# Optimization experiments

Measured on AMD Instinct MI355X. Metric: run time of the kernel, lower is better.

## Reference

```python
import jax, jax.numpy as jnp
import numpy as np

B, N, H, F_IN, F_OUT = 16, 512, 8, 128, 128
NEG_SLOPE = 0.2


def setup_inputs() -> dict:
    key = jax.random.key(0)
    k_h, k_adj, k_bias, k_W, k_a = jax.random.split(key, 5)
    h = jax.random.normal(k_h, (B, N, F_IN), dtype=jnp.float32)
    # Binary adjacency (shared across batch); force self-loops so every row
    # of the masked softmax has at least one valid entry (avoids NaN rows).
    adj = jax.random.randint(k_adj, (N, N), 0, 2, dtype=jnp.int32)
    adj = adj.at[jnp.arange(N), jnp.arange(N)].set(1)
    bias_matrix = jax.random.normal(k_bias, (1, 1, N, N), dtype=jnp.float32)
    # Xavier-uniform-like init for params
    lim_W = float(np.sqrt(6.0 / (F_IN + F_OUT)))
    W = jax.random.uniform(k_W, (H, F_IN, F_OUT), minval=-lim_W, maxval=lim_W, dtype=jnp.float32)
    lim_a = float(np.sqrt(6.0 / (2 * F_OUT + 1)))
    a = jax.random.uniform(k_a, (H, 2 * F_OUT, 1), minval=-lim_a, maxval=lim_a, dtype=jnp.float32)
    return {"h": h, "adj": adj, "bias_matrix": bias_matrix, "W": W, "a": a}


def reference(h, adj, bias_matrix, W, a):
    # h: [B,N,Fin], adj: [N,N] int, bias_matrix: [1,1,N,N], W: [H,Fin,F], a: [H,2F,1]
    f = W.shape[-1]
    h_prime = jnp.einsum('bni,hio->bnho', h, W)  # [B,N,H,F]
    # e[b,i,j,h] = leakyrelu(a_h . concat(h_prime[b,i,h], h_prime[b,j,h]))
    # Decompose a into src/dst halves: identical math, avoids O(B*N*N*H*2F) cat.
    a_src = a[:, :f, 0]  # [H,F]
    a_dst = a[:, f:, 0]  # [H,F]
    s_src = jnp.einsum('bnhf,hf->bnh', h_prime, a_src)  # score contribution of node i
    s_dst = jnp.einsum('bnhf,hf->bnh', h_prime, a_dst)  # score contribution of node j
    e = jax.nn.leaky_relu(s_src[:, :, None, :] + s_dst[:, None, :, :], NEG_SLOPE)  # [B,N,N,H]
    e = e + bias_matrix[0, 0][None, :, :, None]  # bias broadcast over batch & heads
    mask = (adj != 0)[None, :, :, None]  # [1,N,N,1] -> broadcast [B,N,N,H]
    e = jnp.where(mask, e, -jnp.inf)
    attention = jax.nn.softmax(e, axis=2)  # softmax over neighbors j
    h_out = jnp.einsum('bijh,bjhf->bihf', attention, h_prime)  # [B,N,H,F]
    # concat=False -> mean over heads
    return h_out.mean(axis=2)  # [B,N,F]
```

## Files before the change

kernel.cpp:

```cpp
#include <hip/hip_runtime.h>
#include <hip/hip_bf16.h>
#include <string.h>

#define NB 16
#define NN 512
#define NH 8
#define NF 128
#define NEG_SLOPE 0.2f

typedef short bf16x8 __attribute__((ext_vector_type(8)));
typedef float f32x4 __attribute__((ext_vector_type(4)));

__device__ inline unsigned short f2bf(float x) {
    unsigned int u = __float_as_uint(x);
    unsigned int r = (u + 0x7fffu + ((u >> 16) & 1u)) >> 16;
    return (unsigned short)r;
}

__global__ __launch_bounds__(256) void prep_kernel(
    const int* __restrict__ adj, const float* __restrict__ bias,
    const float* __restrict__ W, const float* __restrict__ a,
    float* __restrict__ mb, float* __restrict__ wasrc, float* __restrict__ wadst)
{
    int t = blockIdx.x * 256 + threadIdx.x;
    if (t < NN * NN) mb[t] = (adj[t] != 0) ? bias[t] : -1.0e30f;
    if (t < NH * NF) {
        int hh = t >> 7, i = t & 127;
        const float* wrow = W + (hh * NF + i) * NF;
        const float* asr = a + hh * 2 * NF;
        const float* ads = asr + NF;
        float s1 = 0.f, s2 = 0.f;
        #pragma unroll 4
        for (int f = 0; f < NF; ++f) {
            float w = wrow[f];
            s1 = fmaf(w, asr[f], s1);
            s2 = fmaf(w, ads[f], s2);
        }
        wasrc[t] = s1; wadst[t] = s2;
    }
}

__global__ __launch_bounds__(256) void score_kernel(
    const float* __restrict__ h, const float* __restrict__ wasrc,
    const float* __restrict__ wadst, float* __restrict__ ssrc, float* __restrict__ sdstT)
{
    __shared__ float wsm[2][NH * (NF + 4)];
    int tid = threadIdx.x;
    for (int u = tid; u < NH * NF; u += 256) {
        int hh = u >> 7, f = u & 127;
        wsm[0][hh * (NF + 4) + f] = wasrc[u];
        wsm[1][hh * (NF + 4) + f] = wadst[u];
    }
    __syncthreads();
    int t = blockIdx.x * 256 + tid;
    int hh = t & 7;
    int bn = t >> 3;
    int b = bn >> 9, n = bn & 511;
    const float4* hrow = (const float4*)(h + (size_t)bn * NF);
    const float4* w1 = (const float4*)(&wsm[0][hh * (NF + 4)]);
    const float4* w2 = (const float4*)(&wsm[1][hh * (NF + 4)]);
    float s1 = 0.f, s2 = 0.f;
    #pragma unroll
    for (int u = 0; u < NF / 4; ++u) {
        float4 hv = hrow[u], a1 = w1[u], a2 = w2[u];
        s1 += hv.x * a1.x + hv.y * a1.y + hv.z * a1.z + hv.w * a1.w;
        s2 += hv.x * a2.x + hv.y * a2.y + hv.z * a2.z + hv.w * a2.w;
    }
    ssrc[t] = s1;
    sdstT[((size_t)(b * NH + hh)) * NN + n] = s2;
}

__global__ __launch_bounds__(256) void hprime_kernel(
    const float* __restrict__ h, const float* __restrict__ W, unsigned short* __restrict__ hpT)
{
    __shared__ float As[64][NF + 4];
    __shared__ float Ws[NF][64];
    int tid = threadIdx.x;
    int rowBase = blockIdx.x * 64;
    int colBase = blockIdx.y * 64;
    int hh = colBase >> 7;
    int fbase = colBase & 127;
    {
        int r = tid >> 2, kc = (tid & 3) * 32;
        const float4* src = (const float4*)(h + (size_t)(rowBase + r) * NF + kc);
        #pragma unroll
        for (int u = 0; u < 8; ++u)
            *(float4*)&As[r][kc + 4 * u] = src[u];
    }
    {
        int c = (tid & 15) * 4;
        int k0 = tid >> 4;
        #pragma unroll
        for (int u = 0; u < 8; ++u) {
            int k = k0 + u * 16;
            *(float4*)&Ws[k][c] = *(const float4*)(W + (size_t)(hh * NF + k) * NF + fbase + c);
        }
    }
    __syncthreads();
    int tx = tid & 15, ty = tid >> 4;
    float acc[4][4];
    #pragma unroll
    for (int r = 0; r < 4; ++r)
        #pragma unroll
        for (int c = 0; c < 4; ++c) acc[r][c] = 0.f;
    #pragma unroll 4
    for (int k = 0; k < NF; ++k) {
        float4 wv = *(const float4*)&Ws[k][tx * 4];
        float av[4];
        av[0] = As[ty * 4 + 0][k];
        av[1] = As[ty * 4 + 1][k];
        av[2] = As[ty * 4 + 2][k];
        av[3] = As[ty * 4 + 3][k];
        #pragma unroll
        for (int r = 0; r < 4; ++r) {
            acc[r][0] = fmaf(av[r], wv.x, acc[r][0]);
            acc[r][1] = fmaf(av[r], wv.y, acc[r][1]);
            acc[r][2] = fmaf(av[r], wv.z, acc[r][2]);
            acc[r][3] = fmaf(av[r], wv.w, acc[r][3]);
        }
    }
    int b = rowBase >> 9;
    int nInB = (rowBase & 511) + ty * 4;
    #pragma unroll
    for (int cc = 0; cc < 4; ++cc) {
        int f = fbase + tx * 4 + cc;
        ushort4 u;
        u.x = f2bf(acc[0][cc]);
        u.y = f2bf(acc[1][cc]);
        u.z = f2bf(acc[2][cc]);
        u.w = f2bf(acc[3][cc]);
        *(ushort4*)&hpT[((size_t)(b * NH + hh) * NF + f) * NN + nInB] = u;
    }
}

__global__ __launch_bounds__(1024, 4) void attn_kernel(
    const unsigned short* __restrict__ hpT, const float* __restrict__ mb,
    const float* __restrict__ ssrc, const float* __restrict__ sdstT,
    float* __restrict__ out)
{
    __shared__ float mbs[32][NN];
    __shared__ unsigned short P[32][NN + 8];

    int i0 = (blockIdx.x & 15) * 32;
    int b  = blockIdx.x >> 4;
    int tid = threadIdx.x;
    int lane = tid & 63, wave = tid >> 6;

    for (int u = tid; u < 32 * (NN / 4); u += 1024) {
        int r = u >> 7, c4 = (u & 127) * 4;
        *(float4*)&mbs[r][c4] = *(const float4*)&mb[(size_t)(i0 + r) * NN + c4];
    }
    __syncthreads();

    int iGrp = wave >> 3;
    int fch  = wave & 7;
    f32x4 acc0 = {0.f, 0.f, 0.f, 0.f};
    f32x4 acc1 = {0.f, 0.f, 0.f, 0.f};

    for (int hh = 0; hh < NH; ++hh) {
        const float* sd = sdstT + ((size_t)(b * NH + hh)) * NN;
        #pragma unroll
        for (int rr = 0; rr < 2; ++rr) {
            int i = wave * 2 + rr;
            int row = i0 + i;
            float s_i = ssrc[((size_t)(b * NN + row)) * NH + hh];
            float p8[8];
            float mx = -3.0e38f;
            #pragma unroll
            for (int v = 0; v < 8; ++v) {
                int j = lane + 64 * v;
                float x = s_i + sd[j];
                x = x > 0.f ? x : NEG_SLOPE * x;
                float e = x + mbs[i][j];
                p8[v] = e;
                mx = fmaxf(mx, e);
            }
            #pragma unroll
            for (int off = 32; off; off >>= 1) mx = fmaxf(mx, __shfl_xor(mx, off));
            float sum = 0.f;
            #pragma unroll
            for (int v = 0; v < 8; ++v) { p8[v] = __expf(p8[v] - mx); sum += p8[v]; }
            #pragma unroll
            for (int off = 32; off; off >>= 1) sum += __shfl_xor(sum, off);
            float rinv = 1.0f / sum;
            #pragma unroll
            for (int v = 0; v < 8; ++v)
                P[i][lane + 64 * v] = f2bf(p8[v] * rinv);
        }
        __syncthreads();

        const unsigned short* Bp = hpT
            + ((size_t)(b * NH + hh) * NF + fch * 16 + (lane & 15)) * NN
            + (lane >> 4) * 8;
        const unsigned short* Ap = &P[iGrp * 16 + (lane & 15)][(lane >> 4) * 8];
        #pragma unroll
        for (int ks = 0; ks < 16; ks += 2) {
            bf16x8 a0 = *(const bf16x8*)(Ap + ks * 32);
            bf16x8 b0 = *(const bf16x8*)(Bp + ks * 32);
            acc0 = __builtin_amdgcn_mfma_f32_16x16x32_bf16(a0, b0, acc0, 0, 0, 0);
            bf16x8 a1 = *(const bf16x8*)(Ap + (ks + 1) * 32);
            bf16x8 b1 = *(const bf16x8*)(Bp + (ks + 1) * 32);
            acc1 = __builtin_amdgcn_mfma_f32_16x16x32_bf16(a1, b1, acc1, 0, 0, 0);
        }
        __syncthreads();
    }

    int f = fch * 16 + (lane & 15);
    int ibase = i0 + iGrp * 16 + (lane >> 4) * 4;
    #pragma unroll
    for (int r = 0; r < 4; ++r)
        out[((size_t)(b * NN + ibase + r)) * NF + f] = (acc0[r] + acc1[r]) * 0.125f;
}

extern "C" void kernel_launch(void* const* d_in, const int* in_sizes, int n_in,
                              void* d_out, int out_size, void* d_ws, size_t ws_size,
                              hipStream_t stream)
{
    const float* h    = (const float*)d_in[0];
    const int*   adj  = (const int*)d_in[1];
    const float* bias = (const float*)d_in[2];
    const float* W    = (const float*)d_in[3];
    const float* a    = (const float*)d_in[4];
    float* out = (float*)d_out;

    unsigned short* hpT = (unsigned short*)d_ws;
    float* mb    = (float*)(hpT + (size_t)NB * NH * NF * NN);
    float* ssrc  = mb + (size_t)NN * NN;
    float* sdstT = ssrc + (size_t)NB * NN * NH;
    float* wasrc = sdstT + (size_t)NB * NN * NH;
    float* wadst = wasrc + NH * NF;

    hipLaunchKernelGGL(prep_kernel, dim3((NN * NN) / 256), dim3(256), 0, stream,
                       adj, bias, W, a, mb, wasrc, wadst);
    hipLaunchKernelGGL(score_kernel, dim3((NB * NN * NH) / 256), dim3(256), 0, stream,
                       h, wasrc, wadst, ssrc, sdstT);
    hipLaunchKernelGGL(hprime_kernel, dim3((NB * NN) / 64, (NH * NF) / 64), dim3(256), 0, stream,
                       h, W, hpT);
    hipLaunchKernelGGL(attn_kernel, dim3(NB * (NN / 32)), dim3(1024), 0, stream,
                       hpT, mb, ssrc, sdstT, out);
}
```

Before: 193.3 us.

## Use split-bf16 MFMA for h' projection and split attention over head halves

Adds a split kernel that stores h and transposed W as hi/lo bf16 pairs. The h' projection now runs as three-pass bf16 MFMA (hi*hi, lo*hi, hi*lo) instead of a scalar fp32 FMA GEMM, which shifts that compute onto the matrix cores. The attention kernel now uses 16-row tiles with 512 threads, splits the 8 heads across two blocks that write partial sums, and loads the bias/mask directly from global with vectorized reads instead of staging it in LDS. It also prefetches B fragments and adds a combine kernel, which costs two extra launches and extra global traffic for the hi/lo buffers and the partial outputs.

```diff
diff --git a/kernel.cpp b/kernel.cpp
--- a/kernel.cpp
+++ b/kernel.cpp
@@ -1,6 +1,5 @@
 #include <hip/hip_runtime.h>
 #include <hip/hip_bf16.h>
-#include <string.h>
 
 #define NB 16
 #define NN 512
@@ -9,12 +8,16 @@
 #define NEG_SLOPE 0.2f
 
 typedef short bf16x8 __attribute__((ext_vector_type(8)));
+typedef unsigned short u16x8 __attribute__((ext_vector_type(8)));
 typedef float f32x4 __attribute__((ext_vector_type(4)));
 
 __device__ inline unsigned short f2bf(float x) {
     unsigned int u = __float_as_uint(x);
     unsigned int r = (u + 0x7fffu + ((u >> 16) & 1u)) >> 16;
     return (unsigned short)r;
+}
+__device__ inline float bf2f(unsigned short u) {
+    return __uint_as_float(((unsigned int)u) << 16);
 }
 
 __global__ __launch_bounds__(256) void prep_kernel(
@@ -40,6 +43,29 @@
     }
 }
 
+__global__ __launch_bounds__(256) void split_kernel(
+    const float* __restrict__ h, const float* __restrict__ W,
+    unsigned short* __restrict__ hHi, unsigned short* __restrict__ hLo,
+    unsigned short* __restrict__ wtHi, unsigned short* __restrict__ wtLo)
+{
+    int t = blockIdx.x * 256 + threadIdx.x;
+    if (t < NB * NN * NF) {
+        float v = h[t];
+        unsigned short hi = f2bf(v);
+        hHi[t] = hi;
+        hLo[t] = f2bf(v - bf2f(hi));
+    } else {
+        int u = t - NB * NN * NF;
+        if (u < NH * NF * NF) {
+            int fg = u >> 7, k = u & 127;
+            float v = W[(size_t)(fg >> 7) * NF * NF + k * NF + (fg & 127)];
+            unsigned short hi = f2bf(v);
+            wtHi[u] = hi;
+            wtLo[u] = f2bf(v - bf2f(hi));
+        }
+    }
+}
+
 __global__ __launch_bounds__(256) void score_kernel(
     const float* __restrict__ h, const float* __restrict__ wasrc,
     const float* __restrict__ wadst, float* __restrict__ ssrc, float* __restrict__ sdstT)
@@ -71,110 +97,114 @@
 }
 
 __global__ __launch_bounds__(256) void hprime_kernel(
-    const float* __restrict__ h, const float* __restrict__ W, unsigned short* __restrict__ hpT)
-{
-    __shared__ float As[64][NF + 4];
-    __shared__ float Ws[NF][64];
+    const unsigned short* __restrict__ hHi, const unsigned short* __restrict__ hLo,
+    const unsigned short* __restrict__ wtHi, const unsigned short* __restrict__ wtLo,
+    unsigned short* __restrict__ hpT)
+{
     int tid = threadIdx.x;
-    int rowBase = blockIdx.x * 64;
-    int colBase = blockIdx.y * 64;
-    int hh = colBase >> 7;
-    int fbase = colBase & 127;
-    {
-        int r = tid >> 2, kc = (tid & 3) * 32;
-        const float4* src = (const float4*)(h + (size_t)(rowBase + r) * NF + kc);
-        #pragma unroll
-        for (int u = 0; u < 8; ++u)
-            *(float4*)&As[r][kc + 4 * u] = src[u];
-    }
-    {
-        int c = (tid & 15) * 4;
-        int k0 = tid >> 4;
-        #pragma unroll
-        for (int u = 0; u < 8; ++u) {
-            int k = k0 + u * 16;
-            *(float4*)&Ws[k][c] = *(const float4*)(W + (size_t)(hh * NF + k) * NF + fbase + c);
-        }
-    }
-    __syncthreads();
-    int tx = tid & 15, ty = tid >> 4;
-    float acc[4][4];
+    int wave = tid >> 6, lane = tid & 63;
+    int col = lane & 15, kg = lane >> 4;
+    int f0 = blockIdx.y * 64 + wave * 16;
+    int n0 = blockIdx.x * 64;
+
+    const unsigned short* Ah = wtHi + (size_t)(f0 + col) * NF + kg * 8;
+    const unsigned short* Al = wtLo + (size_t)(f0 + col) * NF + kg * 8;
+    const unsigned short* Bh0 = hHi + (size_t)(n0 +  0 + col) * NF + kg * 8;
+    const unsigned short* Bh1 = hHi + (size_t)(n0 + 16 + col) * NF + kg * 8;
+    const unsigned short* Bh2 = hHi + (size_t)(n0 + 32 + col) * NF + kg * 8;
+    const unsigned short* Bh3 = hHi + (size_t)(n0 + 48 + col) * NF + kg * 8;
+    const unsigned short* Bl0 = hLo + (size_t)(n0 +  0 + col) * NF + kg * 8;
+    const unsigned short* Bl1 = hLo + (size_t)(n0 + 16 + col) * NF + kg * 8;
+    const unsigned short* Bl2 = hLo + (size_t)(n0 + 32 + col) * NF + kg * 8;
+    const unsigned short* Bl3 = hLo + (size_t)(n0 + 48 + col) * NF + kg * 8;
+
+    f32x4 acc0 = {0.f,0.f,0.f,0.f}, acc1 = {0.f,0.f,0.f,0.f};
+    f32x4 acc2 = {0.f,0.f,0.f,0.f}, acc3 = {0.f,0.f,0.f,0.f};
+
     #pragma unroll
-    for (int r = 0; r < 4; ++r)
-        #pragma unroll
-        for (int c = 0; c < 4; ++c) acc[r][c] = 0.f;
-    #pragma unroll 4
-    for (int k = 0; k < NF; ++k) {
-        float4 wv = *(const float4*)&Ws[k][tx * 4];
-        float av[4];
-        av[0] = As[ty * 4 + 0][k];
-        av[1] = As[ty * 4 + 1][k];
-        av[2] = As[ty * 4 + 2][k];
-        av[3] = As[ty * 4 + 3][k];
-        #pragma unroll
-        for (int r = 0; r < 4; ++r) {
-            acc[r][0] = fmaf(av[r], wv.x, acc[r][0]);
-            acc[r][1] = fmaf(av[r], wv.y, acc[r][1]);
-            acc[r][2] = fmaf(av[r], wv.z, acc[r][2]);
-            acc[r][3] = fmaf(av[r], wv.w, acc[r][3]);
-        }
-    }
-    int b = rowBase >> 9;
-    int nInB = (rowBase & 511) + ty * 4;
+    for (int ks = 0; ks < 4; ++ks) {
+        int off = ks * 32;
+        bf16x8 ahi = *(const bf16x8*)(Ah + off);
+        bf16x8 alo = *(const bf16x8*)(Al + off);
+        bf16x8 b0h = *(const bf16x8*)(Bh0 + off);
+        bf16x8 b1h = *(const bf16x8*)(Bh1 + off);
+        bf16x8 b2h = *(const bf16x8*)(Bh2 + off);
+        bf16x8 b3h = *(const bf16x8*)(Bh3 + off);
+        bf16x8 b0l = *(const bf16x8*)(Bl0 + off);
+        bf16x8 b1l = *(const bf16x8*)(Bl1 + off);
+        bf16x8 b2l = *(const bf16x8*)(Bl2 + off);
+        bf16x8 b3l = *(const bf16x8*)(Bl3 + off);
+        acc0 = __builtin_amdgcn_mfma_f32_16x16x32_bf16(ahi, b0h, acc0, 0, 0, 0);
+        acc1 = __builtin_amdgcn_mfma_f32_16x16x32_bf16(ahi, b1h, acc1, 0, 0, 0);
+        acc2 = __builtin_amdgcn_mfma_f32_16x16x32_bf16(ahi, b2h, acc2, 0, 0, 0);
+        acc3 = __builtin_amdgcn_mfma_f32_16x16x32_bf16(ahi, b3h, acc3, 0, 0, 0);
+        acc0 = __builtin_amdgcn_mfma_f32_16x16x32_bf16(alo, b0h, acc0, 0, 0, 0);
+        acc1 = __builtin_amdgcn_mfma_f32_16x16x32_bf16(alo, b1h, acc1, 0, 0, 0);
+        acc2 = __builtin_amdgcn_mfma_f32_16x16x32_bf16(alo, b2h, acc2, 0, 0, 0);
+        acc3 = __builtin_amdgcn_mfma_f32_16x16x32_bf16(alo, b3h, acc3, 0, 0, 0);
+        acc0 = __builtin_amdgcn_mfma_f32_16x16x32_bf16(ahi, b0l, acc0, 0, 0, 0);
+        acc1 = __builtin_amdgcn_mfma_f32_16x16x32_bf16(ahi, b1l, acc1, 0, 0, 0);
+        acc2 = __builtin_amdgcn_mfma_f32_16x16x32_bf16(ahi, b2l, acc2, 0, 0, 0);
+        acc3 = __builtin_amdgcn_mfma_f32_16x16x32_bf16(ahi, b3l, acc3, 0, 0, 0);
+    }
+
+    int b = n0 >> 9;
+    int nin = n0 & 511;
     #pragma unroll
-    for (int cc = 0; cc < 4; ++cc) {
-        int f = fbase + tx * 4 + cc;
-        ushort4 u;
-        u.x = f2bf(acc[0][cc]);
-        u.y = f2bf(acc[1][cc]);
-        u.z = f2bf(acc[2][cc]);
-        u.w = f2bf(acc[3][cc]);
-        *(ushort4*)&hpT[((size_t)(b * NH + hh) * NF + f) * NN + nInB] = u;
-    }
-}
-
-__global__ __launch_bounds__(1024, 4) void attn_kernel(
+    for (int r = 0; r < 4; ++r) {
+        int fg = f0 + kg * 4 + r;
+        size_t base = ((size_t)b * (NH * NF) + fg) * NN + nin + col;
+        hpT[base +  0] = f2bf(acc0[r]);
+        hpT[base + 16] = f2bf(acc1[r]);
+        hpT[base + 32] = f2bf(acc2[r]);
+        hpT[base + 48] = f2bf(acc3[r]);
+    }
+}
+
+__global__ __launch_bounds__(512, 8) void attn_kernel(
     const unsigned short* __restrict__ hpT, const float* __restrict__ mb,
     const float* __restrict__ ssrc, const float* __restrict__ sdstT,
-    float* __restrict__ out)
-{
-    __shared__ float mbs[32][NN];
-    __shared__ unsigned short P[32][NN + 8];
-
-    int i0 = (blockIdx.x & 15) * 32;
-    int b  = blockIdx.x >> 4;
+    float* __restrict__ part)
+{
+    __shared__ unsigned short P[16][520];
+
+    int bx = blockIdx.x;
+    int half = bx & 1;
+    int it = (bx >> 1) & 31;
+    int b = bx >> 6;
+    int i0 = it * 16;
     int tid = threadIdx.x;
     int lane = tid & 63, wave = tid >> 6;
-
-    for (int u = tid; u < 32 * (NN / 4); u += 1024) {
-        int r = u >> 7, c4 = (u & 127) * 4;
-        *(float4*)&mbs[r][c4] = *(const float4*)&mb[(size_t)(i0 + r) * NN + c4];
-    }
-    __syncthreads();
-
-    int iGrp = wave >> 3;
-    int fch  = wave & 7;
-    f32x4 acc0 = {0.f, 0.f, 0.f, 0.f};
-    f32x4 acc1 = {0.f, 0.f, 0.f, 0.f};
-
-    for (int hh = 0; hh < NH; ++hh) {
-        const float* sd = sdstT + ((size_t)(b * NH + hh)) * NN;
+    int col = lane & 15, kg = lane >> 4;
+
+    f32x4 acc0 = {0.f,0.f,0.f,0.f}, acc1 = {0.f,0.f,0.f,0.f};
+
+    for (int hq = 0; hq < 4; ++hq) {
+        int head = half * 4 + hq;
+        const float* sd = sdstT + (size_t)(b * NH + head) * NN;
         #pragma unroll
         for (int rr = 0; rr < 2; ++rr) {
             int i = wave * 2 + rr;
             int row = i0 + i;
-            float s_i = ssrc[((size_t)(b * NN + row)) * NH + hh];
+            float s_i = ssrc[((size_t)(b * NN + row)) * NH + head];
+            const float4* sd4 = (const float4*)(sd + lane * 8);
+            const float4* mb4 = (const float4*)(mb + (size_t)row * NN + lane * 8);
+            float4 sv0 = sd4[0], sv1 = sd4[1];
+            float4 mv0 = mb4[0], mv1 = mb4[1];
             float p8[8];
-            float mx = -3.0e38f;
-            #pragma unroll
-            for (int v = 0; v < 8; ++v) {
-                int j = lane + 64 * v;
-                float x = s_i + sd[j];
-                x = x > 0.f ? x : NEG_SLOPE * x;
-                float e = x + mbs[i][j];
-                p8[v] = e;
-                mx = fmaxf(mx, e);
+            {
+                float x;
+                x = s_i + sv0.x; x = x > 0.f ? x : NEG_SLOPE * x; p8[0] = x + mv0.x;
+                x = s_i + sv0.y; x = x > 0.f ? x : NEG_SLOPE * x; p8[1] = x + mv0.y;
+                x = s_i + sv0.z; x = x > 0.f ? x : NEG_SLOPE * x; p8[2] = x + mv0.z;
+                x = s_i + sv0.w; x = x > 0.f ? x : NEG_SLOPE * x; p8[3] = x + mv0.w;
+                x = s_i + sv1.x; x = x > 0.f ? x : NEG_SLOPE * x; p8[4] = x + mv1.x;
+                x = s_i + sv1.y; x = x > 0.f ? x : NEG_SLOPE * x; p8[5] = x + mv1.y;
+                x = s_i + sv1.z; x = x > 0.f ? x : NEG_SLOPE * x; p8[6] = x + mv1.z;
+                x = s_i + sv1.w; x = x > 0.f ? x : NEG_SLOPE * x; p8[7] = x + mv1.w;
             }
+            float mx = fmaxf(fmaxf(fmaxf(p8[0], p8[1]), fmaxf(p8[2], p8[3])),
+                             fmaxf(fmaxf(p8[4], p8[5]), fmaxf(p8[6], p8[7])));
             #pragma unroll
             for (int off = 32; off; off >>= 1) mx = fmaxf(mx, __shfl_xor(mx, off));
             float sum = 0.f;
@@ -183,33 +213,53 @@
             #pragma unroll
             for (int off = 32; off; off >>= 1) sum += __shfl_xor(sum, off);
             float rinv = 1.0f / sum;
+            u16x8 pw;
             #pragma unroll
-            for (int v = 0; v < 8; ++v)
-                P[i][lane + 64 * v] = f2bf(p8[v] * rinv);
+            for (int v = 0; v < 8; ++v) pw[v] = f2bf(p8[v] * rinv);
+            *(u16x8*)&P[i][lane * 8] = pw;
         }
         __syncthreads();
 
         const unsigned short* Bp = hpT
-            + ((size_t)(b * NH + hh) * NF + fch * 16 + (lane & 15)) * NN
-            + (lane >> 4) * 8;
-        const unsigned short* Ap = &P[iGrp * 16 + (lane & 15)][(lane >> 4) * 8];
+            + ((size_t)(b * NH + head) * NF + wave * 16 + col) * NN + kg * 8;
+        const unsigned short* Ap = &P[col][kg * 8];
+        bf16x8 B0v = *(const bf16x8*)(Bp);
+        bf16x8 B1v = *(const bf16x8*)(Bp + 32);
         #pragma unroll
-        for (int ks = 0; ks < 16; ks += 2) {
-            bf16x8 a0 = *(const bf16x8*)(Ap + ks * 32);
-            bf16x8 b0 = *(const bf16x8*)(Bp + ks * 32);
-            acc0 = __builtin_amdgcn_mfma_f32_16x16x32_bf16(a0, b0, acc0, 0, 0, 0);
-            bf16x8 a1 = *(const bf16x8*)(Ap + (ks + 1) * 32);
-            bf16x8 b1 = *(const bf16x8*)(Bp + (ks + 1) * 32);
-            acc1 = __builtin_amdgcn_mfma_f32_16x16x32_bf16(a1, b1, acc1, 0, 0, 0);
+        for (int ks = 0; ks < 8; ++ks) {
+            bf16x8 a0 = *(const bf16x8*)(Ap + ks * 64);
+            bf16x8 a1 = *(const bf16x8*)(Ap + ks * 64 + 32);
+            bf16x8 nb0, nb1;
+            if (ks < 7) {
+                nb0 = *(const bf16x8*)(Bp + ks * 64 + 64);
+                nb1 = *(const bf16x8*)(Bp + ks * 64 + 96);
+            }
+            acc0 = __builtin_amdgcn_mfma_f32_16x16x32_bf16(a0, B0v, acc0, 0, 0, 0);
+            acc1 = __builtin_amdgcn_mfma_f32_16x16x32_bf16(a1, B1v, acc1, 0, 0, 0);
+            if (ks < 7) { B0v = nb0; B1v = nb1; }
         }
         __syncthreads();
     }
 
-    int f = fch * 16 + (lane & 15);
-    int ibase = i0 + iGrp * 16 + (lane >> 4) * 4;
+    float* po = part + (size_t)half * (NB * NN * NF);
     #pragma unroll
-    for (int r = 0; r < 4; ++r)
-        out[((size_t)(b * NN + ibase + r)) * NF + f] = (acc0[r] + acc1[r]) * 0.125f;
+    for (int r = 0; r < 4; ++r) {
+        po[((size_t)(b * NN + i0 + kg * 4 + r)) * NF + wave * 16 + col] = acc0[r] + acc1[r];
+    }
+}
+
+__global__ __launch_bounds__(256) void combine_kernel(
+    const float* __restrict__ part, float* __restrict__ out)
+{
+    int t = blockIdx.x * 256 + threadIdx.x;
+    float4 a = ((const float4*)part)[t];
+    float4 c = ((const float4*)(part + (size_t)NB * NN * NF))[t];
+    float4 o;
+    o.x = (a.x + c.x) * 0.125f;
+    o.y = (a.y + c.y) * 0.125f;
+    o.z = (a.z + c.z) * 0.125f;
+    o.w = (a.w + c.w) * 0.125f;
+    ((float4*)out)[t] = o;
 }
 
 extern "C" void kernel_launch(void* const* d_in, const int* in_sizes, int n_in,
@@ -223,19 +273,29 @@
     const float* a    = (const float*)d_in[4];
     float* out = (float*)d_out;
 
-    unsigned short* hpT = (unsigned short*)d_ws;
-    float* mb    = (float*)(hpT + (size_t)NB * NH * NF * NN);
-    float* ssrc  = mb + (size_t)NN * NN;
-    float* sdstT = ssrc + (size_t)NB * NN * NH;
-    float* wasrc = sdstT + (size_t)NB * NN * NH;
-    float* wadst = wasrc + NH * NF;
+    char* ws = (char*)d_ws;
+    unsigned short* hpT  = (unsigned short*)ws;                 ws += (size_t)NB * NH * NF * NN * 2;
+    float* mb    = (float*)ws;                                  ws += (size_t)NN * NN * 4;
+    float* ssrc  = (float*)ws;                                  ws += (size_t)NB * NN * NH * 4;
+    float* sdstT = (float*)ws;                                  ws += (size_t)NB * NN * NH * 4;
+    float* wasrc = (float*)ws;                                  ws += NH * NF * 4;
+    float* wadst = (float*)ws;                                  ws += NH * NF * 4;
+    unsigned short* hHi  = (unsigned short*)ws;                 ws += (size_t)NB * NN * NF * 2;
+    unsigned short* hLo  = (unsigned short*)ws;                 ws += (size_t)NB * NN * NF * 2;
+    unsigned short* wtHi = (unsigned short*)ws;                 ws += (size_t)NH * NF * NF * 2;
+    unsigned short* wtLo = (unsigned short*)ws;                 ws += (size_t)NH * NF * NF * 2;
+    float* part  = (float*)ws;                                  ws += (size_t)2 * NB * NN * NF * 4;
 
     hipLaunchKernelGGL(prep_kernel, dim3((NN * NN) / 256), dim3(256), 0, stream,
                        adj, bias, W, a, mb, wasrc, wadst);
+    hipLaunchKernelGGL(split_kernel, dim3((NB * NN * NF + NH * NF * NF) / 256), dim3(256), 0, stream,
+                       h, W, hHi, hLo, wtHi, wtLo);
     hipLaunchKernelGGL(score_kernel, dim3((NB * NN * NH) / 256), dim3(256), 0, stream,
                        h, wasrc, wadst, ssrc, sdstT);
     hipLaunchKernelGGL(hprime_kernel, dim3((NB * NN) / 64, (NH * NF) / 64), dim3(256), 0, stream,
-                       h, W, hpT);
-    hipLaunchKernelGGL(attn_kernel, dim3(NB * (NN / 32)), dim3(1024), 0, stream,
-                       hpT, mb, ssrc, sdstT, out);
-}
+                       hHi, hLo, wtHi, wtLo, hpT);
+    hipLaunchKernelGGL(attn_kernel, dim3(NB * 32 * 2), dim3(512), 0, stream,
+                       hpT, mb, ssrc, sdstT, part);
+    hipLaunchKernelGGL(combine_kernel, dim3((NB * NN * NF / 4) / 256), dim3(256), 0, stream,
+                       part, out);
+}
```

Measured after the change: 191.0 us. No clear change (-1.2%).
